# Optimization experiments

Hardware: AMD Instinct MI355X
Metric: run time of the kernel (lower is better)

Reference implementation:

```python
import jax, jax.numpy as jnp
import numpy as np

V, H, S, U, UC, E = 30000, 128, 32, 128, 10000, 300000
LAMBDA_T, LAMBDA_S = 0.1, 100.0
DAY = 86400.0


def setup_inputs() -> dict:
    key = jax.random.key(0)
    k = jax.random.split(key, 20)
    sc = 0.02
    x = jax.random.randint(k[0], (S, U), 0, V)
    # timestamps: cumulative positive intervals so t[i] >= t[j] for j <= i
    t = jnp.cumsum(jax.random.uniform(k[1], (S, U), minval=60.0, maxval=3600.0), axis=0)
    t_slot = jax.random.randint(k[2], (S, U), 0, 168)
    s = jax.random.normal(k[3], (S, U, 2)) * 0.1
    y_t = t + 600.0
    y_t_slot = jax.random.randint(k[4], (S, U), 0, 168)
    y_s = jax.random.normal(k[5], (S, U, 2)) * 0.1
    h = jnp.zeros((U, H), jnp.float32)
    active_user = jax.random.randint(k[6], (U,), 0, UC)
    graph_rows = jax.random.randint(k[7], (E,), 0, V)
    graph_cols = jax.random.randint(k[8], (E,), 0, V)
    enc_emb = jax.random.normal(k[9], (V, H)) * sc
    user_emb = jax.random.normal(k[10], (UC, H)) * sc
    pref_emb = jax.random.normal(k[11], (1, 2 * H)) * sc
    proj_W = jax.random.normal(k[12], (H, 2 * H)) * sc
    proj_b = jnp.zeros((2 * H,), jnp.float32)
    W_ih = jax.random.normal(k[13], (H, H)) * sc
    W_hh = jax.random.normal(k[14], (H, H)) * sc
    b_rnn = jnp.zeros((H,), jnp.float32)
    fc_W = jax.random.normal(k[15], (2 * H, V)) * sc
    fc_b = jnp.zeros((V,), jnp.float32)
    return dict(x=x, t=t, t_slot=t_slot, s=s, y_t=y_t, y_t_slot=y_t_slot, y_s=y_s,
                h=h, active_user=active_user, graph_rows=graph_rows, graph_cols=graph_cols,
                enc_emb=enc_emb, user_emb=user_emb, pref_emb=pref_emb,
                proj_W=proj_W, proj_b=proj_b, W_ih=W_ih, W_hh=W_hh, b_rnn=b_rnn,
                fc_W=fc_W, fc_b=fc_b)


def reference(x, t, t_slot, s, y_t, y_t_slot, y_s, h, active_user, graph_rows, graph_cols,
              enc_emb, user_emb, pref_emb, proj_W, proj_b, W_ih, W_hh, b_rnn, fc_W, fc_b):
    # --- random-walk-normalized graph conv: D^{-1}(A + I) @ enc_emb ---
    ones_e = jnp.ones(graph_rows.shape, enc_emb.dtype)
    deg = jax.ops.segment_sum(ones_e, graph_rows, num_segments=V) + 1.0  # +1 self loop
    agg = jax.ops.segment_sum(enc_emb[graph_cols], graph_rows, num_segments=V)
    encoder_weight = (agg + enc_emb) / deg[:, None]  # [V, H]

    x_emb = encoder_weight[x]  # [S, U, H]

    # --- vanilla tanh RNN over the sequence dim ---
    def step(hprev, xt):
        hn = jnp.tanh(xt @ W_ih.T + hprev @ W_hh.T + b_rnn)
        return hn, hn
    h_last, out = jax.lax.scan(step, h, x_emb)  # out: [S, U, H]

    # --- user preference similarity (TransE-style: user + pref vs loc) ---
    p_u = user_emb[active_user]                       # [U, H]
    p_proj = jnp.tanh(p_u @ proj_W + proj_b)          # [U, 2H]
    x_proj = jnp.tanh(x_emb @ proj_W + proj_b)        # [S, U, 2H]
    sim = jax.nn.sigmoid(jnp.einsum('ud,sud->us', p_proj + pref_emb[0], x_proj))  # [U, S]

    # --- causal spatio-temporal decay weighted average (the O(S^2) loop, vectorized) ---
    dist_t = t[:, None, :] - t[None, :, :]                       # [S, S, U] (i, j, u)
    dist_s = jnp.linalg.norm(s[:, None] - s[None, :], axis=-1)   # [S, S, U]
    a = 0.5 * (jnp.cos(dist_t * (2.0 * jnp.pi / DAY)) + 1.0) * jnp.exp(-(dist_t / DAY) * LAMBDA_T)
    b = jnp.exp(-dist_s * LAMBDA_S)
    w = (a * b + 1e-10) * jnp.transpose(sim)[None, :, :]         # scale by sim[u, j]
    causal = jnp.tril(jnp.ones((S, S), w.dtype))
    w = w * causal[:, :, None]
    sum_w = jnp.sum(w, axis=1)                                   # [S, U]
    out_w = jnp.einsum('iju,juh->iuh', w, out) / sum_w[..., None]  # [S, U, H]

    # --- concat user embedding, final projection to location logits ---
    out_pu = jnp.concatenate([out_w, jnp.broadcast_to(p_u, (S, U, H))], axis=-1)  # [S, U, 2H]
    y_linear = out_pu @ fc_W + fc_b  # [S, U, V]
    return y_linear, h_last
```

## Files before the change

### kernel.cpp

```cpp
#include <hip/hip_runtime.h>
#include <hip/hip_bf16.h>

#define VV 30000
#define HH 128
#define SS 32
#define UU 128
#define EE 300000

typedef unsigned short u16;
typedef unsigned int u32;

__device__ __forceinline__ u16 f2b(float f){ union{float f; u32 i;} v; v.f=f; u32 x=v.i; x += 0x7fffu + ((x>>16)&1u); return (u16)(x>>16); }

typedef __bf16 bf16x8 __attribute__((ext_vector_type(8)));
typedef float f32x4 __attribute__((ext_vector_type(4)));

__device__ __forceinline__ void gl_lds16(const void* g, void* l){
  __builtin_amdgcn_global_load_lds((const __attribute__((address_space(1))) u32*)g,
                                   (__attribute__((address_space(3))) u32*)l, 16, 0, 0);
}

__global__ __launch_bounds__(256) void k_flagdeg(const int* __restrict__ x, const int* __restrict__ rows,
    int* __restrict__ needed, int* __restrict__ deg){
  int gid = blockIdx.x*256 + threadIdx.x;
  if (gid < SS*UU) needed[x[gid]] = 1;
  if (gid < EE) atomicAdd(&deg[rows[gid]], 1);
}

__global__ __launch_bounds__(256) void k_agg(const int* __restrict__ rows, const int* __restrict__ cols,
    const float* __restrict__ enc, const int* __restrict__ needed, float* __restrict__ agg){
  int hh  = threadIdx.x & 127;
  int sub = threadIdx.x >> 7;
  int stride = gridDim.x * 2;
  for (int e = blockIdx.x*2 + sub; e < EE; e += stride){
    int r = rows[e];
    if (!needed[r]) continue;
    int c = cols[e];
    atomicAdd(&agg[(size_t)r*HH + hh], enc[(size_t)c*HH + hh]);
  }
}

__global__ __launch_bounds__(128) void k_xemb(const int* __restrict__ x, const float* __restrict__ agg,
    const float* __restrict__ enc, const int* __restrict__ deg, float* __restrict__ xemb){
  int su = blockIdx.x, hh = threadIdx.x;
  int v = x[su];
  float d = (float)(deg[v] + 1);
  xemb[su*HH + hh] = (agg[(size_t)v*HH + hh] + enc[(size_t)v*HH + hh]) / d;
}

__global__ __launch_bounds__(256) void k_rnn(const float* __restrict__ xemb,
     const float* __restrict__ h0, const float* __restrict__ Wih, const float* __restrict__ Whh,
     const float* __restrict__ brnn, float* __restrict__ outws, float* __restrict__ hlast)
{
  int u = blockIdx.x, t = threadIdx.x;
  int d = t & 127, half = t >> 7;
  __shared__ float xbuf[128], hbuf[128], part[256];
  float wf[128];
  const float4* wr4 = (const float4*)((half ? Whh : Wih) + d*HH);
  #pragma unroll
  for(int i=0;i<32;i++){
    float4 q = wr4[i];
    wf[4*i+0]=q.x; wf[4*i+1]=q.y; wf[4*i+2]=q.z; wf[4*i+3]=q.w;
  }
  float bias = 0.f;
  if (t < 128){ hbuf[t] = h0[u*HH + t]; bias = brnn[t]; }
  for(int s0=0; s0<SS; ++s0){
    if (t < 128) xbuf[t] = xemb[(s0*UU + u)*HH + t];
    __syncthreads();
    const float4* vp = (const float4*)(half ? hbuf : xbuf);
    float a0=0.f, a1=0.f, a2=0.f, a3=0.f;
    #pragma unroll
    for(int k4=0;k4<32;k4+=4){
      float4 v0 = vp[k4+0], v1 = vp[k4+1], v2 = vp[k4+2], v3 = vp[k4+3];
      a0 += wf[4*k4+0]*v0.x + wf[4*k4+1]*v0.y + wf[4*k4+2]*v0.z + wf[4*k4+3]*v0.w;
      a1 += wf[4*k4+4]*v1.x + wf[4*k4+5]*v1.y + wf[4*k4+6]*v1.z + wf[4*k4+7]*v1.w;
      a2 += wf[4*k4+8]*v2.x + wf[4*k4+9]*v2.y + wf[4*k4+10]*v2.z + wf[4*k4+11]*v2.w;
      a3 += wf[4*k4+12]*v3.x + wf[4*k4+13]*v3.y + wf[4*k4+14]*v3.z + wf[4*k4+15]*v3.w;
    }
    part[t] = (a0+a1)+(a2+a3);
    __syncthreads();
    if (t < 128){
      float hn = tanhf(part[t] + part[t+128] + bias);
      outws[(s0*UU + u)*HH + t] = hn;
      hbuf[t] = hn;
      if (s0 == SS-1) hlast[u*HH + t] = hn;
    }
    __syncthreads();
  }
}

__global__ __launch_bounds__(256) void k_pproj(const int* __restrict__ au, const float* __restrict__ uemb,
    const float* __restrict__ projW, const float* __restrict__ projb, const float* __restrict__ pref,
    float* __restrict__ sp)
{
  int u = blockIdx.x, d = threadIdx.x;
  __shared__ float pl[128];
  int a = au[u];
  if (d < 128) pl[d] = uemb[(size_t)a*HH + d];
  __syncthreads();
  float acc = 0.f;
  #pragma unroll 4
  for(int k=0;k<128;k++) acc += pl[k]*projW[k*256 + d];
  sp[u*256 + d] = tanhf(acc + projb[d]) + pref[d];
}

__global__ __launch_bounds__(256) void k_xprojsim(const float* __restrict__ xemb,
   const float* __restrict__ projW, const float* __restrict__ projb,
   const float* __restrict__ sp, float* __restrict__ sim)
{
  int su = blockIdx.x; int s0 = su >> 7, u = su & 127;
  int d = threadIdx.x;
  __shared__ float xl[128];
  __shared__ float red[4];
  if (d < 128) xl[d] = xemb[su*HH + d];
  __syncthreads();
  float a0 = 0.f, a1 = 0.f;
  #pragma unroll 4
  for(int k=0;k<128;k+=2){
    a0 += xl[k]*projW[k*256 + d];
    a1 += xl[k+1]*projW[(k+1)*256 + d];
  }
  float xp = tanhf(a0 + a1 + projb[d]);
  float val = xp * sp[u*256 + d];
  for(int off=32; off>0; off>>=1) val += __shfl_down(val, off, 64);
  if ((d & 63) == 0) red[d>>6] = val;
  __syncthreads();
  if (d == 0){
    float sum = red[0]+red[1]+red[2]+red[3];
    sim[u*SS + s0] = 1.f/(1.f + expf(-sum));
  }
}

__global__ __launch_bounds__(256) void k_decay(const float* __restrict__ t_in, const float* __restrict__ s_in,
    const float* __restrict__ sim, const float* __restrict__ outws,
    const float* __restrict__ uemb, const int* __restrict__ au, u16* __restrict__ outpu)
{
  int u = blockIdx.x, tid = threadIdx.x;
  __shared__ float outL[SS*HH];
  __shared__ float wm[SS*SS];
  __shared__ float tl[SS], sx[SS], sy[SS], sml[SS], swv[SS];
  __shared__ u16 pub[HH];
  for(int idx=tid; idx<SS*HH; idx+=256){
    int j = idx >> 7, hh = idx & 127;
    outL[idx] = outws[(j*UU + u)*HH + hh];
  }
  if (tid < SS){
    tl[tid]  = t_in[tid*UU + u];
    sx[tid]  = s_in[(tid*UU + u)*2 + 0];
    sy[tid]  = s_in[(tid*UU + u)*2 + 1];
    sml[tid] = sim[u*SS + tid];
  }
  if (tid < HH) pub[tid] = f2b(uemb[(size_t)au[u]*HH + tid]);
  __syncthreads();
  for(int p=tid; p<SS*SS; p+=256){
    int i = p >> 5, j = p & 31;
    float wv = 0.f;
    if (j <= i){
      float dt = tl[i] - tl[j];
      float a = 0.5f*(cosf(dt * 7.2722052166430399e-05f) + 1.0f) * expf(dt * -1.1574074074074074e-06f);
      float dx = sx[i]-sx[j], dy = sy[i]-sy[j];
      float b = expf(-100.0f * sqrtf(dx*dx + dy*dy));
      wv = (a*b + 1e-10f) * sml[j];
    }
    wm[p] = wv;
  }
  __syncthreads();
  if (tid < SS){
    float ssum = 0.f;
    for(int j=0;j<=tid;j++) ssum += wm[tid*32 + j];
    swv[tid] = ssum;
  }
  __syncthreads();
  for(int p=tid; p<SS*HH; p+=256){
    int i = p >> 7, hh = p & 127;
    float accv = 0.f;
    for(int j=0;j<=i;j++) accv += wm[i*32 + j]*outL[j*128 + hh];
    size_t row = (size_t)(i*UU + u)*256;
    outpu[row + hh] = f2b(accv / swv[i]);
    outpu[row + 128 + hh] = pub[hh];
  }
}

__global__ __launch_bounds__(256) void k_transp(const float* __restrict__ fcW, u16* __restrict__ fcwT){
  __shared__ u16 tl[64*65];
  int n0 = blockIdx.x*64, k0 = blockIdx.y*64;
  int tid = threadIdx.x;
  {
    int nn = tid & 63, k4 = tid >> 6;
    for (int r = 0; r < 16; ++r) {
      int kk = r*4 + k4;
      int n = n0 + nn;
      u16 v = 0;
      if (n < VV) v = f2b(fcW[(size_t)(k0+kk)*VV + n]);
      tl[kk*65 + nn] = v;
    }
  }
  __syncthreads();
  {
    int kk = tid & 63, n4 = tid >> 6;
    for (int r = 0; r < 16; ++r) {
      int nn = r*4 + n4;
      fcwT[(size_t)(n0+nn)*256 + k0 + kk] = tl[kk*65 + nn];
    }
  }
}

__global__ __launch_bounds__(256) void k_gemm(const u16* __restrict__ A, const u16* __restrict__ BT,
    const float* __restrict__ bias, float* __restrict__ C)
{
  __shared__ __align__(16) char As[32768];
  __shared__ __align__(16) char Bs[32768];
  const int tid  = threadIdx.x;
  const int lane = tid & 63;
  const int wv   = tid >> 6;
  const int wr = wv >> 1, wc = wv & 1;
  const int m0 = blockIdx.x * 128;
  const int n0 = blockIdx.y * 128;

  f32x4 acc[16];
  #pragma unroll
  for(int i=0;i<16;i++) acc[i] = (f32x4){0.f,0.f,0.f,0.f};

  const char* Ab = (const char*)A;
  const char* Bb = (const char*)BT;
  const int srow = tid >> 4;
  const int scol = ((tid & 15) ^ srow) << 4;

  const int fr = lane & 15;
  const int kq = lane >> 4;

  for (int kt = 0; kt < 2; ++kt){
    __syncthreads();
    #pragma unroll
    for (int i = 0; i < 8; ++i)
      gl_lds16(Ab + (size_t)(m0 + i*16 + srow)*512 + kt*256 + scol, As + i*4096 + wv*1024);
    #pragma unroll
    for (int i = 0; i < 8; ++i)
      gl_lds16(Bb + (size_t)(n0 + i*16 + srow)*512 + kt*256 + scol, Bs + i*4096 + wv*1024);
    __syncthreads();

    #pragma unroll
    for (int ks = 0; ks < 4; ++ks){
      bf16x8 af[4], bg[4];
      const int p = ((ks*4 + kq) ^ fr) << 4;
      #pragma unroll
      for (int mt = 0; mt < 4; ++mt)
        af[mt] = *(const bf16x8*)(As + (wr*64 + mt*16 + fr)*256 + p);
      #pragma unroll
      for (int nt = 0; nt < 4; ++nt)
        bg[nt] = *(const bf16x8*)(Bs + (wc*64 + nt*16 + fr)*256 + p);
      #pragma unroll
      for (int mt = 0; mt < 4; ++mt)
        #pragma unroll
        for (int nt = 0; nt < 4; ++nt)
          acc[mt*4+nt] = __builtin_amdgcn_mfma_f32_16x16x32_bf16(af[mt], bg[nt], acc[mt*4+nt], 0, 0, 0);
    }
  }

  const int n_base = n0 + wc*64;
  float bl[4];
  #pragma unroll
  for(int nt=0;nt<4;++nt){
    int n = n_base + nt*16 + fr;
    bl[nt] = (n < VV) ? bias[n] : 0.f;
  }
  const bool full = (n0 + 128 <= VV);
  #pragma unroll
  for(int mt=0;mt<4;++mt){
    #pragma unroll
    for(int r=0;r<4;++r){
      size_t rowoff = (size_t)(m0 + wr*64 + mt*16 + kq*4 + r) * VV;
      if (full){
        #pragma unroll
        for(int nt=0;nt<4;++nt)
          __builtin_nontemporal_store(acc[mt*4+nt][r] + bl[nt], &C[rowoff + n_base + nt*16 + fr]);
      } else {
        #pragma unroll
        for(int nt=0;nt<4;++nt){
          int n = n_base + nt*16 + fr;
          if (n < VV) __builtin_nontemporal_store(acc[mt*4+nt][r] + bl[nt], &C[rowoff + n]);
        }
      }
    }
  }
}

extern "C" void kernel_launch(void* const* d_in, const int* in_sizes, int n_in,
                              void* d_out, int out_size, void* d_ws, size_t ws_size,
                              hipStream_t stream)
{
  (void)in_sizes; (void)n_in; (void)out_size; (void)ws_size;
  const int*   x      = (const int*)d_in[0];
  const float* t_in   = (const float*)d_in[1];
  const float* s_in   = (const float*)d_in[3];
  const float* h0     = (const float*)d_in[7];
  const int*   au     = (const int*)d_in[8];
  const int*   grows  = (const int*)d_in[9];
  const int*   gcols  = (const int*)d_in[10];
  const float* enc    = (const float*)d_in[11];
  const float* uemb   = (const float*)d_in[12];
  const float* pref   = (const float*)d_in[13];
  const float* projW  = (const float*)d_in[14];
  const float* projb  = (const float*)d_in[15];
  const float* Wih    = (const float*)d_in[16];
  const float* Whh    = (const float*)d_in[17];
  const float* brnn   = (const float*)d_in[18];
  const float* fcW    = (const float*)d_in[19];
  const float* fcb    = (const float*)d_in[20];
  float* yf = (float*)d_out;
  float* hlast = yf + (size_t)SS*UU*VV;
  char* ws = (char*)d_ws;
  int*   needed = (int*)(ws + 0);
  int*   deg    = (int*)(ws + 120000);
  float* agg    = (float*)(ws + 240000);
  u16*   fcwT   = (u16*)(ws + 0);
  float* xemb   = (float*)(ws + 15600000);
  float* outws  = (float*)(ws + 17697152);
  float* sp     = (float*)(ws + 19794304);
  float* sim    = (float*)(ws + 19925376);
  u16*   outpu  = (u16*)(ws + 19941760);

  hipMemsetAsync(ws, 0, 15600000, stream);
  hipLaunchKernelGGL(k_flagdeg,  dim3(1172),    dim3(256), 0, stream, x, grows, needed, deg);
  hipLaunchKernelGGL(k_agg,      dim3(2048),    dim3(256), 0, stream, grows, gcols, enc, needed, agg);
  hipLaunchKernelGGL(k_xemb,     dim3(SS*UU),   dim3(128), 0, stream, x, agg, enc, deg, xemb);
  hipLaunchKernelGGL(k_transp,   dim3(470,4),   dim3(256), 0, stream, fcW, fcwT);
  hipLaunchKernelGGL(k_rnn,      dim3(UU),      dim3(256), 0, stream, xemb, h0, Wih, Whh, brnn, outws, hlast);
  hipLaunchKernelGGL(k_pproj,    dim3(UU),      dim3(256), 0, stream, au, uemb, projW, projb, pref, sp);
  hipLaunchKernelGGL(k_xprojsim, dim3(SS*UU),   dim3(256), 0, stream, xemb, projW, projb, sp, sim);
  hipLaunchKernelGGL(k_decay,    dim3(UU),      dim3(256), 0, stream, t_in, s_in, sim, outws, uemb, au, outpu);
  hipLaunchKernelGGL(k_gemm,     dim3(32,235),  dim3(256), 0, stream, outpu, fcwT, fcb, yf);
}
```

Baseline: 774.9 us.

## Fuse user/sequence projection kernels and remap GEMM block order

Merges the user-preference projection and the per-step projection plus similarity into one kernel. Each block handles four time steps of one user and reuses each projW load for five dot products, which removes a launch and the intermediate buffer. The GEMM now maps block IDs through a swizzle so that neighbouring workgroups cover different tiles, which may spread them across caches or channels. It also adds a launch bound of two blocks per SM and restructures the two k-stages into lambdas, dropping the first leading barrier. The trade-off is that the fused kernel recomputes the user projection in every block, and the launch bound may limit registers.

```diff
diff --git a/kernel.cpp b/kernel.cpp
--- a/kernel.cpp
+++ b/kernel.cpp
@@ -89,45 +89,47 @@
   }
 }
 
-__global__ __launch_bounds__(256) void k_pproj(const int* __restrict__ au, const float* __restrict__ uemb,
+__global__ __launch_bounds__(256) void k_prefsim(const int* __restrict__ au, const float* __restrict__ uemb,
     const float* __restrict__ projW, const float* __restrict__ projb, const float* __restrict__ pref,
-    float* __restrict__ sp)
-{
-  int u = blockIdx.x, d = threadIdx.x;
+    const float* __restrict__ xemb, float* __restrict__ sim)
+{
+  int bid = blockIdx.x;
+  int u = bid >> 3, s0 = (bid & 7) * 4;
+  int d = threadIdx.x;
   __shared__ float pl[128];
+  __shared__ float xl[4*128];
+  __shared__ float red2[4][4];
   int a = au[u];
   if (d < 128) pl[d] = uemb[(size_t)a*HH + d];
-  __syncthreads();
-  float acc = 0.f;
+  for (int idx = d; idx < 4*128; idx += 256){
+    int si = idx >> 7, k = idx & 127;
+    xl[idx] = xemb[((size_t)(s0+si)*UU + u)*HH + k];
+  }
+  __syncthreads();
+  float accp = 0.f;
+  float acs0 = 0.f, acs1 = 0.f, acs2 = 0.f, acs3 = 0.f;
   #pragma unroll 4
-  for(int k=0;k<128;k++) acc += pl[k]*projW[k*256 + d];
-  sp[u*256 + d] = tanhf(acc + projb[d]) + pref[d];
-}
-
-__global__ __launch_bounds__(256) void k_xprojsim(const float* __restrict__ xemb,
-   const float* __restrict__ projW, const float* __restrict__ projb,
-   const float* __restrict__ sp, float* __restrict__ sim)
-{
-  int su = blockIdx.x; int s0 = su >> 7, u = su & 127;
-  int d = threadIdx.x;
-  __shared__ float xl[128];
-  __shared__ float red[4];
-  if (d < 128) xl[d] = xemb[su*HH + d];
-  __syncthreads();
-  float a0 = 0.f, a1 = 0.f;
-  #pragma unroll 4
-  for(int k=0;k<128;k+=2){
-    a0 += xl[k]*projW[k*256 + d];
-    a1 += xl[k+1]*projW[(k+1)*256 + d];
-  }
-  float xp = tanhf(a0 + a1 + projb[d]);
-  float val = xp * sp[u*256 + d];
-  for(int off=32; off>0; off>>=1) val += __shfl_down(val, off, 64);
-  if ((d & 63) == 0) red[d>>6] = val;
-  __syncthreads();
-  if (d == 0){
-    float sum = red[0]+red[1]+red[2]+red[3];
-    sim[u*SS + s0] = 1.f/(1.f + expf(-sum));
+  for (int k = 0; k < 128; ++k){
+    float w = projW[k*256 + d];
+    accp += pl[k]*w;
+    acs0 += xl[0*128 + k]*w;
+    acs1 += xl[1*128 + k]*w;
+    acs2 += xl[2*128 + k]*w;
+    acs3 += xl[3*128 + k]*w;
+  }
+  float pb = projb[d];
+  float spd = tanhf(accp + pb) + pref[d];
+  float acs[4] = {acs0, acs1, acs2, acs3};
+  #pragma unroll
+  for (int si = 0; si < 4; ++si){
+    float val = tanhf(acs[si] + pb) * spd;
+    for (int off = 32; off > 0; off >>= 1) val += __shfl_down(val, off, 64);
+    if ((d & 63) == 0) red2[si][d >> 6] = val;
+  }
+  __syncthreads();
+  if (d < 4){
+    float sum = red2[d][0] + red2[d][1] + red2[d][2] + red2[d][3];
+    sim[u*SS + s0 + d] = 1.f/(1.f + expf(-sum));
   }
 }
 
@@ -205,7 +207,7 @@
   }
 }
 
-__global__ __launch_bounds__(256) void k_gemm(const u16* __restrict__ A, const u16* __restrict__ BT,
+__global__ __launch_bounds__(256, 2) void k_gemm(const u16* __restrict__ A, const u16* __restrict__ BT,
     const float* __restrict__ bias, float* __restrict__ C)
 {
   __shared__ __align__(16) char As[32768];
@@ -214,8 +216,11 @@
   const int lane = tid & 63;
   const int wv   = tid >> 6;
   const int wr = wv >> 1, wc = wv & 1;
-  const int m0 = blockIdx.x * 128;
-  const int n0 = blockIdx.y * 128;
+
+  const int l  = blockIdx.y * 32 + blockIdx.x;
+  const int wk = (l & 7) * 940 + (l >> 3);
+  const int m0 = (wk & 31) * 128;
+  const int n0 = (wk >> 5) * 128;
 
   f32x4 acc[16];
   #pragma unroll
@@ -229,16 +234,15 @@
   const int fr = lane & 15;
   const int kq = lane >> 4;
 
-  for (int kt = 0; kt < 2; ++kt){
-    __syncthreads();
+  auto STAGE = [&](int kt){
     #pragma unroll
     for (int i = 0; i < 8; ++i)
       gl_lds16(Ab + (size_t)(m0 + i*16 + srow)*512 + kt*256 + scol, As + i*4096 + wv*1024);
     #pragma unroll
     for (int i = 0; i < 8; ++i)
       gl_lds16(Bb + (size_t)(n0 + i*16 + srow)*512 + kt*256 + scol, Bs + i*4096 + wv*1024);
-    __syncthreads();
-
+  };
+  auto COMPUTE = [&](){
     #pragma unroll
     for (int ks = 0; ks < 4; ++ks){
       bf16x8 af[4], bg[4];
@@ -255,7 +259,15 @@
         for (int nt = 0; nt < 4; ++nt)
           acc[mt*4+nt] = __builtin_amdgcn_mfma_f32_16x16x32_bf16(af[mt], bg[nt], acc[mt*4+nt], 0, 0, 0);
     }
-  }
+  };
+
+  STAGE(0);
+  __syncthreads();
+  COMPUTE();
+  __syncthreads();
+  STAGE(1);
+  __syncthreads();
+  COMPUTE();
 
   const int n_base = n0 + wc*64;
   float bl[4];
@@ -316,7 +328,6 @@
   u16*   fcwT   = (u16*)(ws + 0);
   float* xemb   = (float*)(ws + 15600000);
   float* outws  = (float*)(ws + 17697152);
-  float* sp     = (float*)(ws + 19794304);
   float* sim    = (float*)(ws + 19925376);
   u16*   outpu  = (u16*)(ws + 19941760);
 
@@ -326,8 +337,7 @@
   hipLaunchKernelGGL(k_xemb,     dim3(SS*UU),   dim3(128), 0, stream, x, agg, enc, deg, xemb);
   hipLaunchKernelGGL(k_transp,   dim3(470,4),   dim3(256), 0, stream, fcW, fcwT);
   hipLaunchKernelGGL(k_rnn,      dim3(UU),      dim3(256), 0, stream, xemb, h0, Wih, Whh, brnn, outws, hlast);
-  hipLaunchKernelGGL(k_pproj,    dim3(UU),      dim3(256), 0, stream, au, uemb, projW, projb, pref, sp);
-  hipLaunchKernelGGL(k_xprojsim, dim3(SS*UU),   dim3(256), 0, stream, xemb, projW, projb, sp, sim);
+  hipLaunchKernelGGL(k_prefsim,  dim3(UU*8),    dim3(256), 0, stream, au, uemb, projW, projb, pref, xemb, sim);
   hipLaunchKernelGGL(k_decay,    dim3(UU),      dim3(256), 0, stream, t_in, s_in, sim, outws, uemb, au, outpu);
   hipLaunchKernelGGL(k_gemm,     dim3(32,235),  dim3(256), 0, stream, outpu, fcwT, fcb, yf);
 }
```

Result: no change. 764.6 us (-1.3%).
